# Optimization experiments

Measured on AMD Instinct MI355X. Metric: run time of the kernel, lower is better.

Reference implementation:

```python
import jax, jax.numpy as jnp
import numpy as np

K = 5                                   # kernel_sz
SIGMA_SPATIAL = 2.0
SIGMA_INTENSITY = 0.1
NEG_SS_DIV = -1.0 / (2.0 * SIGMA_SPATIAL ** 2.0)   # value stored in self.kernel (same for all K*K taps)
SI_DIV = 1.0 / (2.0 * SIGMA_INTENSITY ** 2.0)      # self.sigma_intensity_div


def setup_inputs() -> dict:
    key = jax.random.key(0)
    k1, k2 = jax.random.split(key)
    t = jax.random.uniform(k1, (2, 3, 720, 1280), dtype=jnp.float32)      # guide image in [0,1]
    vector_curr = jax.random.normal(k2, (2, 2, 720, 1280), dtype=jnp.float32)  # flow vectors
    return {"t": t, "vector_curr": vector_curr}


def _joint_bilateral(t, v):
    # Fused sliding-window formulation: instead of materializing (N,H,W,K^2,C)
    # unfold patches, loop over the K*K static offsets (zero padding = F.unfold default)
    # and accumulate the weighted sum / normalizer. Same math as the original.
    N, C, H, W = t.shape
    Cv = v.shape[1]
    p = K // 2
    tp = jnp.pad(t, ((0, 0), (0, 0), (p, p), (p, p)))
    vp = jnp.pad(v, ((0, 0), (0, 0), (p, p), (p, p)))
    num = jnp.zeros_like(v)                      # (N,Cv,H,W)
    den = jnp.zeros((N, 1, H, W), t.dtype)
    for dy in range(K):
        for dx in range(K):
            ts = jax.lax.slice(tp, (0, 0, dy, dx), (N, C, dy + H, dx + W))
            vs = jax.lax.slice(vp, (0, 0, dy, dx), (N, Cv, dy + H, dx + W))
            # intensity_diff summed over guide channels -> (N,1,H,W)
            intensity_diff = jnp.sum((t - ts) ** 2, axis=1, keepdims=True)
            # coeff = clamp(1 - |kernel - diff * sigma_intensity_div|, 0, 1)
            coeff = jnp.clip(1.0 - jnp.abs(NEG_SS_DIV - intensity_diff * SI_DIV), 0.0, 1.0)
            num = num + vs * coeff
            den = den + coeff
    return (num / den).astype(jnp.float16)       # original returns fp16 NCHW


def reference(t, vector_curr):
    return _joint_bilateral(t, vector_curr)
```

## Files before the change

### kernel.cpp

```cpp
#include <hip/hip_runtime.h>
#include <hip/hip_fp16.h>


constexpr int H_ = 720;
constexpr int W_ = 1280;
constexpr int HW = H_ * W_;
constexpr float COEF0 = 0.875f;
constexpr float SIDIV = 50.0f;

constexpr int TC = 132;
constexpr int TR = 12;
constexpr int NK = 34;
constexpr int NCHUNK = 5 * TR * NK;
constexpr int NXCD = 8;
constexpr int CPX = 1800 / NXCD;

#define LOADW(LR)                                                              \
    float w0[8], w1[8], w2[8], u0[8], u1[8];                                   \
    _Pragma("unroll") for (int s_ = 0; s_ < 2; ++s_) {                         \
        *(float4*)(w0 + 4 * s_) = *(const float4*)&lds[0][LR][lc + 4 * s_];    \
        *(float4*)(w1 + 4 * s_) = *(const float4*)&lds[1][LR][lc + 4 * s_];    \
        *(float4*)(w2 + 4 * s_) = *(const float4*)&lds[2][LR][lc + 4 * s_];    \
        *(float4*)(u0 + 4 * s_) = *(const float4*)&lds[3][LR][lc + 4 * s_];    \
        *(float4*)(u1 + 4 * s_) = *(const float4*)&lds[4][LR][lc + 4 * s_];    \
    }

#define COMPW()                                                                \
    _Pragma("unroll") for (int dx_ = 0; dx_ < 5; ++dx_)                        \
        _Pragma("unroll") for (int j_ = 0; j_ < 4; ++j_) {                     \
            const int k_ = dx_ + j_;                                           \
            const float d0_ = c0f[j_] - w0[k_];                                \
            const float d1_ = c1f[j_] - w1[k_];                                \
            const float d2_ = c2f[j_] - w2[k_];                                \
            float diff_ = d0_ * d0_;                                           \
            diff_ = fmaf(d1_, d1_, diff_);                                     \
            diff_ = fmaf(d2_, d2_, diff_);                                     \
            const float c_ = fmaxf(fmaf(diff_, -SIDIV, COEF0), 0.f);           \
            num0[j_] = fmaf(u0[k_], c_, num0[j_]);                             \
            num1[j_] = fmaf(u1[k_], c_, num1[j_]);                             \
            den[j_] += c_;                                                     \
        }

__global__ __launch_bounds__(256)
void jbf_x(const float* __restrict__ t, const float* __restrict__ v,
           float* __restrict__ out) {
    __shared__ float lds[5][TR][TC];

    const int wgid = (blockIdx.x & (NXCD - 1)) * CPX + (blockIdx.x >> 3);
    const int n   = wgid / 900;
    const int rem = wgid % 900;
    const int by  = rem / 10;
    const int bx  = rem % 10;
    const int gx0 = bx * 128;
    const int gy0 = by * 8;

    const float* tn = t + (size_t)n * 3 * HW;
    const float* vn = v + (size_t)n * 2 * HW;
    float*       on = out + (size_t)n * 2 * HW;

    const int tid = threadIdx.x;

#pragma unroll
    for (int it = 0; it < 8; ++it) {
        const int i = tid + it * 256;
        if (i < NCHUNK) {
            const int k  = i % NK;
            const int rr = (i / NK) % TR;
            const int ch = i / (NK * TR);
            const int gy = gy0 - 2 + rr;
            const int gx = gx0 - 4 + 4 * k;
            float4 val = make_float4(0.f, 0.f, 0.f, 0.f);
            if ((unsigned)gy < (unsigned)H_ && (unsigned)gx < (unsigned)(W_ - 3)) {
                const float* src = (ch < 3) ? (tn + (size_t)ch * HW)
                                            : (vn + (size_t)(ch - 3) * HW);
                val = *(const float4*)(src + gy * W_ + gx);
            }
            float* row = &lds[ch][rr][0];
            if (k > 0)      *(float2*)&row[4 * k - 2] = make_float2(val.x, val.y);
            if (k < NK - 1) *(float2*)&row[4 * k]     = make_float2(val.z, val.w);
        }
    }
    __syncthreads();

    const int tx = tid & 31;
    const int ty = tid >> 5;
    const int lc = 4 * tx;

    float c0f[4], c1f[4], c2f[4];
    float num0[4] = {0.f, 0.f, 0.f, 0.f};
    float num1[4] = {0.f, 0.f, 0.f, 0.f};
    float den[4]  = {0.f, 0.f, 0.f, 0.f};

    {
        const int lr = ty + 2;
        LOADW(lr)
#pragma unroll
        for (int j = 0; j < 4; ++j) {
            c0f[j] = w0[j + 2];
            c1f[j] = w1[j + 2];
            c2f[j] = w2[j + 2];
        }
        COMPW()
    }
#pragma unroll 1
    for (int i = 0; i < 4; ++i) {
        const int r = i + (i >> 1);
        const int lr = ty + r;
        LOADW(lr)
        COMPW()
    }

    float4 o0, o1;
    float* o0a = (float*)&o0;
    float* o1a = (float*)&o1;
#pragma unroll
    for (int j = 0; j < 4; ++j) {
        const float rcp = 1.f / den[j];
        o0a[j] = __half2float(__float2half(num0[j] * rcp));
        o1a[j] = __half2float(__float2half(num1[j] * rcp));
    }
    const int ctr = (gy0 + ty) * W_ + gx0 + 4 * tx;
    *(float4*)(on + ctr) = o0;
    *(float4*)(on + HW + ctr) = o1;
}

extern "C" void kernel_launch(void* const* d_in, const int* in_sizes, int n_in,
                              void* d_out, int out_size, void* d_ws, size_t ws_size,
                              hipStream_t stream) {
    const float* t = (const float*)d_in[0];
    const float* v = (const float*)d_in[1];
    float* out = (float*)d_out;

    jbf_x<<<1800, 256, 0, stream>>>(t, v, out);
}
```

Measured before the change: 27.64 us.

## Store tile in packed fp16 LDS and use fdot2 for intensity differences

Converts the staged guide and flow tiles to fp16 in shared memory, with channels 0/1 and the two flow channels packed as half2 pairs and channel 2 stored separately. The global loads are issued into registers first and converted afterwards. The intensity distance is then computed with a packed fp16 subtract plus fdot2. This halves LDS footprint and read traffic and cuts ALU work per tap, but lowers input precision, which can change the coefficients and the fp16 outputs.

```diff
diff --git a/kernel.cpp b/kernel.cpp
--- a/kernel.cpp
+++ b/kernel.cpp
@@ -1,6 +1,14 @@
 #include <hip/hip_runtime.h>
 #include <hip/hip_fp16.h>
 
+
+typedef _Float16 f16x2 __attribute__((ext_vector_type(2)));
+typedef _Float16 f16x4 __attribute__((ext_vector_type(4)));
+typedef _Float16 f16x8 __attribute__((ext_vector_type(8)));
+
+static __device__ __forceinline__ f16x2 pkrtz(float a, float b) {
+    return __builtin_bit_cast(f16x2, __builtin_amdgcn_cvt_pkrtz(a, b));
+}
 
 constexpr int H_ = 720;
 constexpr int W_ = 1280;
@@ -8,51 +16,26 @@
 constexpr float COEF0 = 0.875f;
 constexpr float SIDIV = 50.0f;
 
-constexpr int TC = 132;
-constexpr int TR = 12;
-constexpr int NK = 34;
-constexpr int NCHUNK = 5 * TR * NK;
+constexpr int TC  = 132;
+constexpr int TCB = 136;
+constexpr int TR  = 12;
+constexpr int NK  = 34;
+constexpr int NITEM = 3 * TR * NK;
 constexpr int NXCD = 8;
 constexpr int CPX = 1800 / NXCD;
 
-#define LOADW(LR)                                                              \
-    float w0[8], w1[8], w2[8], u0[8], u1[8];                                   \
-    _Pragma("unroll") for (int s_ = 0; s_ < 2; ++s_) {                         \
-        *(float4*)(w0 + 4 * s_) = *(const float4*)&lds[0][LR][lc + 4 * s_];    \
-        *(float4*)(w1 + 4 * s_) = *(const float4*)&lds[1][LR][lc + 4 * s_];    \
-        *(float4*)(w2 + 4 * s_) = *(const float4*)&lds[2][LR][lc + 4 * s_];    \
-        *(float4*)(u0 + 4 * s_) = *(const float4*)&lds[3][LR][lc + 4 * s_];    \
-        *(float4*)(u1 + 4 * s_) = *(const float4*)&lds[4][LR][lc + 4 * s_];    \
-    }
-
-#define COMPW()                                                                \
-    _Pragma("unroll") for (int dx_ = 0; dx_ < 5; ++dx_)                        \
-        _Pragma("unroll") for (int j_ = 0; j_ < 4; ++j_) {                     \
-            const int k_ = dx_ + j_;                                           \
-            const float d0_ = c0f[j_] - w0[k_];                                \
-            const float d1_ = c1f[j_] - w1[k_];                                \
-            const float d2_ = c2f[j_] - w2[k_];                                \
-            float diff_ = d0_ * d0_;                                           \
-            diff_ = fmaf(d1_, d1_, diff_);                                     \
-            diff_ = fmaf(d2_, d2_, diff_);                                     \
-            const float c_ = fmaxf(fmaf(diff_, -SIDIV, COEF0), 0.f);           \
-            num0[j_] = fmaf(u0[k_], c_, num0[j_]);                             \
-            num1[j_] = fmaf(u1[k_], c_, num1[j_]);                             \
-            den[j_] += c_;                                                     \
-        }
-
 __global__ __launch_bounds__(256)
-void jbf_x(const float* __restrict__ t, const float* __restrict__ v,
-           float* __restrict__ out) {
-    __shared__ float lds[5][TR][TC];
+void jbf_h2(const float* __restrict__ t, const float* __restrict__ v,
+            float* __restrict__ out) {
+    __shared__ alignas(16) f16x2    ldsA[TR][TC];
+    __shared__ alignas(16) _Float16 ldsB[TR][TCB];
+    __shared__ alignas(16) f16x2    ldsC[TR][TC];
 
     const int wgid = (blockIdx.x & (NXCD - 1)) * CPX + (blockIdx.x >> 3);
     const int n   = wgid / 900;
     const int rem = wgid % 900;
-    const int by  = rem / 10;
-    const int bx  = rem % 10;
-    const int gx0 = bx * 128;
-    const int gy0 = by * 8;
+    const int gy0 = (rem / 10) * 8;
+    const int gx0 = (rem % 10) * 128;
 
     const float* tn = t + (size_t)n * 3 * HW;
     const float* vn = v + (size_t)n * 2 * HW;
@@ -60,24 +43,63 @@
 
     const int tid = threadIdx.x;
 
+    float4 pA[5], pB[5];
 #pragma unroll
-    for (int it = 0; it < 8; ++it) {
+    for (int it = 0; it < 5; ++it) {
+        const int i  = tid + it * 256;
+        const int st = i / 408;
+        const int idx = i % 408;
+        const int rr = idx / 34, k = idx % 34;
+        const int gy = gy0 - 2 + rr;
+        const int gx = gx0 - 4 + 4 * k;
+        pA[it] = make_float4(0.f, 0.f, 0.f, 0.f);
+        pB[it] = make_float4(0.f, 0.f, 0.f, 0.f);
+        const bool live = (it < 4 || i < NITEM) &&
+                          ((unsigned)gy < (unsigned)H_) &&
+                          ((unsigned)gx < (unsigned)(W_ - 3));
+        if (live) {
+            const float* base = tn + gy * W_ + gx;
+            if (st == 0) {
+                pA[it] = *(const float4*)(base);
+                pB[it] = *(const float4*)(base + HW);
+            } else if (st == 1) {
+                pA[it] = *(const float4*)(base + 2 * HW);
+            } else {
+                const float* vb = vn + gy * W_ + gx;
+                pA[it] = *(const float4*)(vb);
+                pB[it] = *(const float4*)(vb + HW);
+            }
+        }
+    }
+
+#pragma unroll
+    for (int it = 0; it < 5; ++it) {
         const int i = tid + it * 256;
-        if (i < NCHUNK) {
-            const int k  = i % NK;
-            const int rr = (i / NK) % TR;
-            const int ch = i / (NK * TR);
-            const int gy = gy0 - 2 + rr;
-            const int gx = gx0 - 4 + 4 * k;
-            float4 val = make_float4(0.f, 0.f, 0.f, 0.f);
-            if ((unsigned)gy < (unsigned)H_ && (unsigned)gx < (unsigned)(W_ - 3)) {
-                const float* src = (ch < 3) ? (tn + (size_t)ch * HW)
-                                            : (vn + (size_t)(ch - 3) * HW);
-                val = *(const float4*)(src + gy * W_ + gx);
+        if (it < 4 || i < NITEM) {
+            const int st = i / 408;
+            const int idx = i % 408;
+            const int rr = idx / 34, k = idx % 34;
+            const float4 a = pA[it], b = pB[it];
+            if (st == 1) {
+                const f16x2 q0 = pkrtz(a.x, a.y);
+                const f16x2 q1 = pkrtz(a.z, a.w);
+                if (k > 0)      *(f16x2*)&ldsB[rr][4 * k - 2] = q0;
+                if (k < NK - 1) *(f16x2*)&ldsB[rr][4 * k]     = q1;
+            } else {
+                const f16x2 p0 = pkrtz(a.x, b.x);
+                const f16x2 p1 = pkrtz(a.y, b.y);
+                const f16x2 p2 = pkrtz(a.z, b.z);
+                const f16x2 p3 = pkrtz(a.w, b.w);
+                f16x2 (*dst)[TC] = (st == 0) ? ldsA : ldsC;
+                if (k > 0) {
+                    f16x4 lo = {p0.x, p0.y, p1.x, p1.y};
+                    *(f16x4*)&dst[rr][4 * k - 2] = lo;
+                }
+                if (k < NK - 1) {
+                    f16x4 hi = {p2.x, p2.y, p3.x, p3.y};
+                    *(f16x4*)&dst[rr][4 * k] = hi;
+                }
             }
-            float* row = &lds[ch][rr][0];
-            if (k > 0)      *(float2*)&row[4 * k - 2] = make_float2(val.x, val.y);
-            if (k < NK - 1) *(float2*)&row[4 * k]     = make_float2(val.z, val.w);
         }
     }
     __syncthreads();
@@ -86,25 +108,53 @@
     const int ty = tid >> 5;
     const int lc = 4 * tx;
 
-    float c0f[4], c1f[4], c2f[4];
     float num0[4] = {0.f, 0.f, 0.f, 0.f};
     float num1[4] = {0.f, 0.f, 0.f, 0.f};
     float den[4]  = {0.f, 0.f, 0.f, 0.f};
+    f16x2 c01[4];
+    float c2f[4];
+
+#define LOADW(LR)                                                              \
+    f16x2 a01[8]; f16x2 uv[8]; float w2f[8];                                   \
+    {                                                                          \
+        *(f16x8*)&a01[0] = *(const f16x8*)&ldsA[LR][lc];                       \
+        *(f16x8*)&a01[4] = *(const f16x8*)&ldsA[LR][lc + 4];                   \
+        f16x4 b0 = *(const f16x4*)&ldsB[LR][lc];                               \
+        f16x4 b1 = *(const f16x4*)&ldsB[LR][lc + 4];                           \
+        *(f16x8*)&uv[0] = *(const f16x8*)&ldsC[LR][lc];                        \
+        *(f16x8*)&uv[4] = *(const f16x8*)&ldsC[LR][lc + 4];                    \
+        _Pragma("unroll") for (int m_ = 0; m_ < 4; ++m_) {                     \
+            w2f[m_]     = (float)b0[m_];                                       \
+            w2f[m_ + 4] = (float)b1[m_];                                       \
+        }                                                                      \
+    }
+
+#define COMPW()                                                                \
+    _Pragma("unroll") for (int dx_ = 0; dx_ < 5; ++dx_)                        \
+        _Pragma("unroll") for (int j_ = 0; j_ < 4; ++j_) {                     \
+            const int k_ = dx_ + j_;                                           \
+            const f16x2 d01 = a01[k_] - c01[j_];                               \
+            const float d2  = w2f[k_] - c2f[j_];                               \
+            const float diff = __builtin_amdgcn_fdot2(d01, d01, d2 * d2, false);\
+            const float c_ = fmaxf(fmaf(diff, -SIDIV, COEF0), 0.f);            \
+            num0[j_] = fmaf((float)uv[k_].x, c_, num0[j_]);                    \
+            num1[j_] = fmaf((float)uv[k_].y, c_, num1[j_]);                    \
+            den[j_] += c_;                                                     \
+        }
 
     {
         const int lr = ty + 2;
         LOADW(lr)
 #pragma unroll
         for (int j = 0; j < 4; ++j) {
-            c0f[j] = w0[j + 2];
-            c1f[j] = w1[j + 2];
-            c2f[j] = w2[j + 2];
+            c01[j] = a01[j + 2];
+            c2f[j] = w2f[j + 2];
         }
         COMPW()
     }
 #pragma unroll 1
-    for (int i = 0; i < 4; ++i) {
-        const int r = i + (i >> 1);
+    for (int i2 = 0; i2 < 4; ++i2) {
+        const int r = i2 + (i2 >> 1);
         const int lr = ty + r;
         LOADW(lr)
         COMPW()
@@ -131,5 +181,5 @@
     const float* v = (const float*)d_in[1];
     float* out = (float*)d_out;
 
-    jbf_x<<<1800, 256, 0, stream>>>(t, v, out);
+    jbf_h2<<<1800, 256, 0, stream>>>(t, v, out);
 }
```

New measurement: 26.08 us. 5.7% less time.
